# Optimization experiments

Measured on AMD Instinct MI355X. Metric: run time of the kernel, lower is better.

## Reference

```python
import jax, jax.numpy as jnp
import numpy as np

D = 256
NUMS_BC = np.array([10, 10, 10]) + 1
NUMS_SC = np.array([10, 10, 10, 10]) + 1
STARTS_BC = jnp.asarray(np.concatenate([[0], np.cumsum(NUMS_BC)[:-1]]))
STARTS_SC = jnp.asarray(np.concatenate([[0], np.cumsum(NUMS_SC)[:-1]]))


def _ln(x, g, b, eps=1e-5):
    mu = x.mean(-1, keepdims=True)
    var = ((x - mu) ** 2).mean(-1, keepdims=True)
    return (x - mu) * jax.lax.rsqrt(var + eps) * g + b


def _cate(x, table, starts, g, b):
    # x: [..., F] int; offset each feature column into its slice of the shared table
    idx = x + 1 + starts
    return _ln(table[idx].sum(-2), g, b)


def setup_inputs():
    key = jax.random.key(0)
    ks = jax.random.split(key, 12)
    B, N, E = 128, 48, 64
    s = 0.02
    return {
        "bond_index": jax.random.randint(ks[0], (B, 2, E), 0, N),
        "bond_feat_cate": jax.random.randint(ks[1], (B, E, 3), 0, 10),
        "bond_feat_float": jax.random.normal(ks[2], (B, E, 4)),
        "bond_mask": jnp.ones((B, E), jnp.float32),
        "structure_feat_cate": jax.random.randint(ks[3], (B, N, N, 4), 0, 10),
        "structure_feat_float": jax.random.normal(ks[4], (B, N, N, 8)),
        "table_bc": jax.random.normal(ks[5], (int(NUMS_BC.sum()), D)) * s,
        "ln_bc_g": jnp.ones((D,)), "ln_bc_b": jnp.zeros((D,)),
        "W_bf": jax.random.normal(ks[6], (4, D)) * s, "b_bf": jnp.zeros((D,)),
        "ln_bf_g": jnp.ones((D,)), "ln_bf_b": jnp.zeros((D,)),
        "table_sc": jax.random.normal(ks[7], (int(NUMS_SC.sum()), D)) * s,
        "ln_sc_g": jnp.ones((D,)), "ln_sc_b": jnp.zeros((D,)),
        "W_sf": jax.random.normal(ks[8], (8, D)) * s, "b_sf": jnp.zeros((D,)),
        "ln_sf_g": jnp.ones((D,)), "ln_sf_b": jnp.zeros((D,)),
        "virtual_edge_emb": jax.random.normal(ks[9], (D,)),
        "W_rev": jax.random.normal(ks[10], (D, D)) * s, "b_rev": jnp.zeros((D,)),
    }


def reference(bond_index, bond_feat_cate, bond_feat_float, bond_mask,
              structure_feat_cate, structure_feat_float,
              table_bc, ln_bc_g, ln_bc_b, W_bf, b_bf, ln_bf_g, ln_bf_b,
              table_sc, ln_sc_g, ln_sc_b, W_sf, b_sf, ln_sf_g, ln_sf_b,
              virtual_edge_emb, W_rev, b_rev):
    B, N = structure_feat_cate.shape[:2]
    M = N + 1  # +1 virtual node
    # per-bond embedding: cate-embed sum + linear float embed, both layernormed
    hb = _cate(bond_feat_cate, table_bc, STARTS_BC, ln_bc_g, ln_bc_b) \
         + _ln(bond_feat_float @ W_bf + b_bf, ln_bf_g, ln_bf_b)
    hb = hb * bond_mask[..., None]  # [B,E,D]
    # dense pairwise structure embedding for real-node block
    block = _cate(structure_feat_cate, table_sc, STARTS_SC, ln_sc_g, ln_sc_b) \
            + _ln(structure_feat_float @ W_sf + b_sf, ln_sf_g, ln_sf_b)  # [B,N,N,D]
    hs = jnp.zeros((B, M, M, hb.shape[-1]), hb.dtype)
    hs = hs.at[:, 0, :, :].set(virtual_edge_emb)
    hs = hs.at[:, :, 0, :].set(virtual_edge_emb)
    hs = hs.at[:, 1:, 1:, :].set(block)
    # scatter-add bond embeddings into (i,j) and reversed projection into (j,i)
    bi = bond_index + 1  # shift past virtual node
    br = jnp.arange(B)[:, None]
    hs = hs.at[br, bi[:, 0], bi[:, 1]].add(hb)
    hs = hs.at[br, bi[:, 1], bi[:, 0]].add(hb @ W_rev + b_rev)
    return hs
```

## Files before the change

### kernel.cpp

```cpp
#include <hip/hip_runtime.h>


#define DD 256
#define BB 128
#define NN 48
#define MM 49
#define EE 64

typedef unsigned long long u64;

__device__ __forceinline__ void wred2(float& s, float& q) {
#pragma unroll
    for (int off = 32; off > 0; off >>= 1) {
        s += __shfl_xor(s, off, 64);
        q += __shfl_xor(q, off, 64);
    }
}

__device__ __forceinline__ void ln4(float& x0, float& x1, float& x2, float& x3,
                                    const float* __restrict__ g,
                                    const float* __restrict__ bb, int d0) {
    float s = x0 + x1 + x2 + x3;
    float q = x0 * x0 + x1 * x1 + x2 * x2 + x3 * x3;
    wred2(s, q);
    float mu  = s * (1.0f / 256.0f);
    float var = q * (1.0f / 256.0f) - mu * mu;
    float rs  = rsqrtf(var + 1e-5f);
    float4 gv = *(const float4*)(g + d0);
    float4 bv = *(const float4*)(bb + d0);
    x0 = (x0 - mu) * rs * gv.x + bv.x;
    x1 = (x1 - mu) * rs * gv.y + bv.y;
    x2 = (x2 - mu) * rs * gv.z + bv.z;
    x3 = (x3 - mu) * rs * gv.w + bv.w;
}

__global__ __launch_bounds__(64) void k_masks(const int* __restrict__ bond_index,
                                              u64* __restrict__ maskA,
                                              u64* __restrict__ maskB) {
    const int b = blockIdx.x;
    const int e = threadIdx.x;
    const int bi0 = bond_index[b * 2 * EE + e];
    const int bi1 = bond_index[b * 2 * EE + EE + e];
    for (int i = 0; i < NN; ++i) {
        u64 mA = __ballot(bi0 == i);
        u64 mB = __ballot(bi1 == i);
        if (e == 0) {
            maskA[b * MM + i + 1] = mA;
            maskB[b * MM + i + 1] = mB;
        }
    }
}

__global__ __launch_bounds__(256) void k_bonds(
    const int* __restrict__ bfc, const float* __restrict__ bff,
    const float* __restrict__ bmask,
    const float* __restrict__ table_bc,
    const float* __restrict__ g_bc, const float* __restrict__ be_bc,
    const float* __restrict__ W_bf, const float* __restrict__ b_bf,
    const float* __restrict__ g_bf, const float* __restrict__ be_bf,
    const float* __restrict__ W_rev, const float* __restrict__ b_rev,
    float* __restrict__ hb_out, float* __restrict__ hbrev_out) {
    __shared__ float hb_lds[16][DD];
    const int blk   = blockIdx.x;
    const int b     = blk >> 2;
    const int group = blk & 3;
    const int tid   = threadIdx.x;
    const int wave  = tid >> 6;
    const int lane  = tid & 63;
    const int d0    = lane << 2;

#pragma unroll
    for (int q = 0; q < 4; ++q) {
        const int el = wave * 4 + q;
        const int be = b * EE + group * 16 + el;

        const int* fc = bfc + be * 3;
        const int i0 = fc[0] + 1;
        const int i1 = fc[1] + 12;
        const int i2 = fc[2] + 23;
        float4 r0 = *(const float4*)(table_bc + i0 * DD + d0);
        float4 r1 = *(const float4*)(table_bc + i1 * DD + d0);
        float4 r2 = *(const float4*)(table_bc + i2 * DD + d0);
        float x0 = r0.x + r1.x + r2.x;
        float x1 = r0.y + r1.y + r2.y;
        float x2 = r0.z + r1.z + r2.z;
        float x3 = r0.w + r1.w + r2.w;
        ln4(x0, x1, x2, x3, g_bc, be_bc, d0);

        float4 fr = *(const float4*)(bff + be * 4);
        float4 w0 = *(const float4*)(W_bf + 0 * DD + d0);
        float4 w1 = *(const float4*)(W_bf + 1 * DD + d0);
        float4 w2 = *(const float4*)(W_bf + 2 * DD + d0);
        float4 w3 = *(const float4*)(W_bf + 3 * DD + d0);
        float4 bb = *(const float4*)(b_bf + d0);
        float y0 = bb.x + fr.x * w0.x + fr.y * w1.x + fr.z * w2.x + fr.w * w3.x;
        float y1 = bb.y + fr.x * w0.y + fr.y * w1.y + fr.z * w2.y + fr.w * w3.y;
        float y2 = bb.z + fr.x * w0.z + fr.y * w1.z + fr.z * w2.z + fr.w * w3.z;
        float y3 = bb.w + fr.x * w0.w + fr.y * w1.w + fr.z * w2.w + fr.w * w3.w;
        ln4(y0, y1, y2, y3, g_bf, be_bf, d0);

        const float m = bmask[be];
        const float h0 = (x0 + y0) * m;
        const float h1 = (x1 + y1) * m;
        const float h2 = (x2 + y2) * m;
        const float h3 = (x3 + y3) * m;

        *(float4*)&hb_lds[el][d0] = make_float4(h0, h1, h2, h3);
        *(float4*)(hb_out + (size_t)be * DD + d0) = make_float4(h0, h1, h2, h3);
    }
    __syncthreads();

    const int d = tid;
    const float brv = b_rev[d];
    float acc[16];
#pragma unroll
    for (int e = 0; e < 16; ++e) acc[e] = brv;
    for (int k = 0; k < DD; k += 4) {
        const float w0 = W_rev[(k + 0) * DD + d];
        const float w1 = W_rev[(k + 1) * DD + d];
        const float w2 = W_rev[(k + 2) * DD + d];
        const float w3 = W_rev[(k + 3) * DD + d];
#pragma unroll
        for (int e = 0; e < 16; ++e) {
            float4 h = *(const float4*)&hb_lds[e][k];
            acc[e] += h.x * w0 + h.y * w1 + h.z * w2 + h.w * w3;
        }
    }
    const int be0 = b * EE + group * 16;
#pragma unroll
    for (int e = 0; e < 16; ++e) {
        hbrev_out[(size_t)(be0 + e) * DD + d] = acc[e];
    }
}

__global__ __launch_bounds__(256) void k_cells(
    const int* __restrict__ sfc, const float* __restrict__ sff,
    const float* __restrict__ table_sc,
    const float* __restrict__ g_sc, const float* __restrict__ be_sc,
    const float* __restrict__ W_sf, const float* __restrict__ b_sf,
    const float* __restrict__ g_sf, const float* __restrict__ be_sf,
    const float* __restrict__ vee,
    const u64* __restrict__ maskA, const u64* __restrict__ maskB,
    const float* __restrict__ hb, const float* __restrict__ hbrev,
    float* __restrict__ out) {
    const int wave = threadIdx.x >> 6;
    const int lane = threadIdx.x & 63;
    const int cell = blockIdx.x * 4 + wave;
    const int b = cell / (MM * MM);
    const int r = cell - b * (MM * MM);
    const int i = r / MM;
    const int j = r - i * MM;
    const int d0 = lane << 2;
    float* op = out + (size_t)cell * DD + d0;

    if (i == 0 || j == 0) {
        *(float4*)op = *(const float4*)(vee + d0);
        return;
    }

    const int ii = i - 1, jj = j - 1;
    const int cidx = (b * NN + ii) * NN + jj;

    const int4 fc = *(const int4*)(sfc + cidx * 4);
    float4 r0 = *(const float4*)(table_sc + (fc.x + 1)  * DD + d0);
    float4 r1 = *(const float4*)(table_sc + (fc.y + 12) * DD + d0);
    float4 r2 = *(const float4*)(table_sc + (fc.z + 23) * DD + d0);
    float4 r3 = *(const float4*)(table_sc + (fc.w + 34) * DD + d0);
    float x0 = r0.x + r1.x + r2.x + r3.x;
    float x1 = r0.y + r1.y + r2.y + r3.y;
    float x2 = r0.z + r1.z + r2.z + r3.z;
    float x3 = r0.w + r1.w + r2.w + r3.w;
    ln4(x0, x1, x2, x3, g_sc, be_sc, d0);

    const float* fp = sff + (size_t)cidx * 8;
    float4 fa = *(const float4*)fp;
    float4 fb = *(const float4*)(fp + 4);
    float f[8] = {fa.x, fa.y, fa.z, fa.w, fb.x, fb.y, fb.z, fb.w};
    float4 bbv = *(const float4*)(b_sf + d0);
    float y0 = bbv.x, y1 = bbv.y, y2 = bbv.z, y3 = bbv.w;
#pragma unroll
    for (int ff = 0; ff < 8; ++ff) {
        float4 wr = *(const float4*)(W_sf + ff * DD + d0);
        y0 += f[ff] * wr.x;
        y1 += f[ff] * wr.y;
        y2 += f[ff] * wr.z;
        y3 += f[ff] * wr.w;
    }
    ln4(y0, y1, y2, y3, g_sf, be_sf, d0);

    float h0 = x0 + y0, h1 = x1 + y1, h2 = x2 + y2, h3 = x3 + y3;

    const u64 mAi = maskA[b * MM + i];
    const u64 mBj = maskB[b * MM + j];
    const u64 mBi = maskB[b * MM + i];
    const u64 mAj = maskA[b * MM + j];
    u64 fwd = mAi & mBj;
    u64 rev = mBi & mAj;
    while (fwd) {
        const int e = __builtin_ctzll(fwd); fwd &= fwd - 1;
        float4 hv = *(const float4*)(hb + (size_t)(b * EE + e) * DD + d0);
        h0 += hv.x; h1 += hv.y; h2 += hv.z; h3 += hv.w;
    }
    while (rev) {
        const int e = __builtin_ctzll(rev); rev &= rev - 1;
        float4 hv = *(const float4*)(hbrev + (size_t)(b * EE + e) * DD + d0);
        h0 += hv.x; h1 += hv.y; h2 += hv.z; h3 += hv.w;
    }

    *(float4*)op = make_float4(h0, h1, h2, h3);
}

extern "C" void kernel_launch(void* const* d_in, const int* in_sizes, int n_in,
                              void* d_out, int out_size, void* d_ws, size_t ws_size,
                              hipStream_t stream) {
    const int*   bond_index = (const int*)d_in[0];
    const int*   bfc        = (const int*)d_in[1];
    const float* bff        = (const float*)d_in[2];
    const float* bmask      = (const float*)d_in[3];
    const int*   sfc        = (const int*)d_in[4];
    const float* sff        = (const float*)d_in[5];
    const float* table_bc   = (const float*)d_in[6];
    const float* g_bc       = (const float*)d_in[7];
    const float* be_bc      = (const float*)d_in[8];
    const float* W_bf       = (const float*)d_in[9];
    const float* b_bf       = (const float*)d_in[10];
    const float* g_bf       = (const float*)d_in[11];
    const float* be_bf      = (const float*)d_in[12];
    const float* table_sc   = (const float*)d_in[13];
    const float* g_sc       = (const float*)d_in[14];
    const float* be_sc      = (const float*)d_in[15];
    const float* W_sf       = (const float*)d_in[16];
    const float* b_sf       = (const float*)d_in[17];
    const float* g_sf       = (const float*)d_in[18];
    const float* be_sf      = (const float*)d_in[19];
    const float* vee        = (const float*)d_in[20];
    const float* W_rev      = (const float*)d_in[21];
    const float* b_rev      = (const float*)d_in[22];

    float* out = (float*)d_out;

    float* hb    = (float*)d_ws;
    float* hbrev = hb + (size_t)BB * EE * DD;
    u64*   maskA = (u64*)(hbrev + (size_t)BB * EE * DD);
    u64*   maskB = maskA + BB * MM;

    k_masks<<<BB, 64, 0, stream>>>(bond_index, maskA, maskB);
    k_bonds<<<BB * 4, 256, 0, stream>>>(bfc, bff, bmask, table_bc, g_bc, be_bc,
                                        W_bf, b_bf, g_bf, be_bf, W_rev, b_rev,
                                        hb, hbrev);
    k_cells<<<(BB * MM * MM) / 4, 256, 0, stream>>>(sfc, sff, table_sc, g_sc, be_sc,
                                                    W_sf, b_sf, g_sf, be_sf, vee,
                                                    maskA, maskB, hb, hbrev, out);
}
```

Before: 579.1 us.

## Precompute layernorm stats via Gram matrices and process seven cells per wave

```diff
diff --git a/kernel.cpp b/kernel.cpp
--- a/kernel.cpp
+++ b/kernel.cpp
@@ -6,8 +6,16 @@
 #define NN 48
 #define MM 49
 #define EE 64
+#define NSC 44
+#define NSF 9
 
 typedef unsigned long long u64;
+
+__device__ __forceinline__ float wredsum(float s) {
+#pragma unroll
+    for (int off = 32; off > 0; off >>= 1) s += __shfl_xor(s, off, 64);
+    return s;
+}
 
 __device__ __forceinline__ void wred2(float& s, float& q) {
 #pragma unroll
@@ -49,6 +57,87 @@
             maskB[b * MM + i + 1] = mB;
         }
     }
+}
+
+__global__ __launch_bounds__(256) void k_prep_means(const float* __restrict__ table_sc,
+                                                    const float* __restrict__ W_sf,
+                                                    const float* __restrict__ b_sf,
+                                                    float* __restrict__ m_sc,
+                                                    float* __restrict__ m_sf) {
+    const int w = (blockIdx.x * 256 + threadIdx.x) >> 6;
+    const int lane = threadIdx.x & 63;
+    if (w >= NSC + NSF) return;
+    const float* src = (w < NSC) ? table_sc + w * DD
+                     : (w == NSC) ? b_sf
+                                  : W_sf + (w - NSC - 1) * DD;
+    float4 v = *(const float4*)(src + lane * 4);
+    float s = wredsum(v.x + v.y + v.z + v.w);
+    if (lane == 0) {
+        if (w < NSC) m_sc[w] = s * (1.0f / 256.0f);
+        else         m_sf[w - NSC] = s * (1.0f / 256.0f);
+    }
+}
+
+__global__ __launch_bounds__(256) void k_prep_gram(const float* __restrict__ table_sc,
+                                                   const float* __restrict__ W_sf,
+                                                   const float* __restrict__ b_sf,
+                                                   const float* __restrict__ m_sc,
+                                                   const float* __restrict__ m_sf,
+                                                   float* __restrict__ G_sc,
+                                                   float* __restrict__ G_sf) {
+    const int w = (blockIdx.x * 256 + threadIdx.x) >> 6;
+    const int lane = threadIdx.x & 63;
+    if (w < NSC * NSC) {
+        const int a = w / NSC, c = w - a * NSC;
+        float4 va = *(const float4*)(table_sc + a * DD + lane * 4);
+        float4 vc = *(const float4*)(table_sc + c * DD + lane * 4);
+        float s = wredsum(va.x * vc.x + va.y * vc.y + va.z * vc.z + va.w * vc.w);
+        if (lane == 0) G_sc[w] = s * (1.0f / 256.0f) - m_sc[a] * m_sc[c];
+    } else if (w < NSC * NSC + NSF * NSF) {
+        const int p = w - NSC * NSC;
+        const int a = p / NSF, c = p - a * NSF;
+        const float* ra = (a == 0) ? b_sf : W_sf + (a - 1) * DD;
+        const float* rc = (c == 0) ? b_sf : W_sf + (c - 1) * DD;
+        float4 va = *(const float4*)(ra + lane * 4);
+        float4 vc = *(const float4*)(rc + lane * 4);
+        float s = wredsum(va.x * vc.x + va.y * vc.y + va.z * vc.z + va.w * vc.w);
+        if (lane == 0) G_sf[p] = s * (1.0f / 256.0f) - m_sf[a] * m_sf[c];
+    }
+}
+
+__global__ __launch_bounds__(256) void k_prep_cells(const int* __restrict__ sfc,
+                                                    const float* __restrict__ sff,
+                                                    const float* __restrict__ m_sc,
+                                                    const float* __restrict__ G_sc,
+                                                    const float* __restrict__ m_sf,
+                                                    const float* __restrict__ G_sf,
+                                                    float4* __restrict__ cellp) {
+    const int c = blockIdx.x * 256 + threadIdx.x;
+    const int4 fc = *(const int4*)(sfc + (size_t)c * 4);
+    int r[4] = {fc.x + 1, fc.y + 12, fc.z + 23, fc.w + 34};
+    float mu_c = m_sc[r[0]] + m_sc[r[1]] + m_sc[r[2]] + m_sc[r[3]];
+    float var_c = 0.f;
+#pragma unroll
+    for (int a = 0; a < 4; ++a)
+#pragma unroll
+        for (int d = 0; d < 4; ++d) var_c += G_sc[r[a] * NSC + r[d]];
+
+    float f[NSF];
+    f[0] = 1.f;
+    float4 fa = *(const float4*)(sff + (size_t)c * 8);
+    float4 fb = *(const float4*)(sff + (size_t)c * 8 + 4);
+    f[1] = fa.x; f[2] = fa.y; f[3] = fa.z; f[4] = fa.w;
+    f[5] = fb.x; f[6] = fb.y; f[7] = fb.z; f[8] = fb.w;
+    float mu_f = 0.f, var_f = 0.f;
+#pragma unroll
+    for (int k = 0; k < NSF; ++k) {
+        mu_f += f[k] * m_sf[k];
+        float t = 0.f;
+#pragma unroll
+        for (int l = 0; l < NSF; ++l) t += f[l] * G_sf[k * NSF + l];
+        var_f += f[k] * t;
+    }
+    cellp[c] = make_float4(mu_c, rsqrtf(var_c + 1e-5f), mu_f, rsqrtf(var_f + 1e-5f));
 }
 
 __global__ __launch_bounds__(256) void k_bonds(
@@ -142,72 +231,97 @@
     const float* __restrict__ vee,
     const u64* __restrict__ maskA, const u64* __restrict__ maskB,
     const float* __restrict__ hb, const float* __restrict__ hbrev,
+    const float4* __restrict__ cellp,
     float* __restrict__ out) {
-    const int wave = threadIdx.x >> 6;
     const int lane = threadIdx.x & 63;
-    const int cell = blockIdx.x * 4 + wave;
-    const int b = cell / (MM * MM);
-    const int r = cell - b * (MM * MM);
-    const int i = r / MM;
-    const int j = r - i * MM;
     const int d0 = lane << 2;
-    float* op = out + (size_t)cell * DD + d0;
-
-    if (i == 0 || j == 0) {
-        *(float4*)op = *(const float4*)(vee + d0);
+    const int wid = __builtin_amdgcn_readfirstlane(blockIdx.x * 4 + (threadIdx.x >> 6));
+    const int b  = wid / (MM * 7);
+    const int rr = wid - b * (MM * 7);
+    const int i  = rr / 7;
+    const int jc = rr - i * 7;
+    const int j0 = jc * 7;
+
+    const float4 veev = *(const float4*)(vee + d0);
+    float* orow = out + (((size_t)b * MM + i) * MM + j0) * DD + d0;
+
+    if (i == 0) {
+#pragma unroll
+        for (int jj = 0; jj < 7; ++jj) *(float4*)(orow + jj * DD) = veev;
         return;
     }
 
-    const int ii = i - 1, jj = j - 1;
-    const int cidx = (b * NN + ii) * NN + jj;
-
-    const int4 fc = *(const int4*)(sfc + cidx * 4);
-    float4 r0 = *(const float4*)(table_sc + (fc.x + 1)  * DD + d0);
-    float4 r1 = *(const float4*)(table_sc + (fc.y + 12) * DD + d0);
-    float4 r2 = *(const float4*)(table_sc + (fc.z + 23) * DD + d0);
-    float4 r3 = *(const float4*)(table_sc + (fc.w + 34) * DD + d0);
-    float x0 = r0.x + r1.x + r2.x + r3.x;
-    float x1 = r0.y + r1.y + r2.y + r3.y;
-    float x2 = r0.z + r1.z + r2.z + r3.z;
-    float x3 = r0.w + r1.w + r2.w + r3.w;
-    ln4(x0, x1, x2, x3, g_sc, be_sc, d0);
-
-    const float* fp = sff + (size_t)cidx * 8;
-    float4 fa = *(const float4*)fp;
-    float4 fb = *(const float4*)(fp + 4);
-    float f[8] = {fa.x, fa.y, fa.z, fa.w, fb.x, fb.y, fb.z, fb.w};
-    float4 bbv = *(const float4*)(b_sf + d0);
-    float y0 = bbv.x, y1 = bbv.y, y2 = bbv.z, y3 = bbv.w;
-#pragma unroll
-    for (int ff = 0; ff < 8; ++ff) {
-        float4 wr = *(const float4*)(W_sf + ff * DD + d0);
-        y0 += f[ff] * wr.x;
-        y1 += f[ff] * wr.y;
-        y2 += f[ff] * wr.z;
-        y3 += f[ff] * wr.w;
-    }
-    ln4(y0, y1, y2, y3, g_sf, be_sf, d0);
-
-    float h0 = x0 + y0, h1 = x1 + y1, h2 = x2 + y2, h3 = x3 + y3;
+    const float4 gsc  = *(const float4*)(g_sc + d0);
+    const float4 bsc  = *(const float4*)(be_sc + d0);
+    const float4 gsf  = *(const float4*)(g_sf + d0);
+    const float4 bsf2 = *(const float4*)(be_sf + d0);
+    const float4 bsf  = *(const float4*)(b_sf + d0);
+    float4 w[8];
+#pragma unroll
+    for (int k = 0; k < 8; ++k) w[k] = *(const float4*)(W_sf + k * DD + d0);
 
     const u64 mAi = maskA[b * MM + i];
-    const u64 mBj = maskB[b * MM + j];
     const u64 mBi = maskB[b * MM + i];
-    const u64 mAj = maskA[b * MM + j];
-    u64 fwd = mAi & mBj;
-    u64 rev = mBi & mAj;
-    while (fwd) {
-        const int e = __builtin_ctzll(fwd); fwd &= fwd - 1;
-        float4 hv = *(const float4*)(hb + (size_t)(b * EE + e) * DD + d0);
-        h0 += hv.x; h1 += hv.y; h2 += hv.z; h3 += hv.w;
-    }
-    while (rev) {
-        const int e = __builtin_ctzll(rev); rev &= rev - 1;
-        float4 hv = *(const float4*)(hbrev + (size_t)(b * EE + e) * DD + d0);
-        h0 += hv.x; h1 += hv.y; h2 += hv.z; h3 += hv.w;
-    }
-
-    *(float4*)op = make_float4(h0, h1, h2, h3);
+    const float* hbB = hb    + ((size_t)b * EE) * DD + d0;
+    const float* hrB = hbrev + ((size_t)b * EE) * DD + d0;
+    const int rowbase = (b * NN + (i - 1)) * NN - 1;
+
+    for (int jj = 0; jj < 7; ++jj) {
+        const int j = j0 + jj;
+        float* op = orow + jj * DD;
+        if (j == 0) { *(float4*)op = veev; continue; }
+
+        const int cidx = rowbase + j;
+        const int4 fc  = *(const int4*)(sfc + (size_t)cidx * 4);
+        const float4 p = cellp[cidx];
+        const float4 t0 = *(const float4*)(table_sc + (fc.x + 1)  * DD + d0);
+        const float4 t1 = *(const float4*)(table_sc + (fc.y + 12) * DD + d0);
+        const float4 t2 = *(const float4*)(table_sc + (fc.z + 23) * DD + d0);
+        const float4 t3 = *(const float4*)(table_sc + (fc.w + 34) * DD + d0);
+        const float4 fa  = *(const float4*)(sff + (size_t)cidx * 8);
+        const float4 fbv = *(const float4*)(sff + (size_t)cidx * 8 + 4);
+
+        float x0 = t0.x + t1.x + t2.x + t3.x;
+        float x1 = t0.y + t1.y + t2.y + t3.y;
+        float x2 = t0.z + t1.z + t2.z + t3.z;
+        float x3 = t0.w + t1.w + t2.w + t3.w;
+        x0 = (x0 - p.x) * p.y * gsc.x + bsc.x;
+        x1 = (x1 - p.x) * p.y * gsc.y + bsc.y;
+        x2 = (x2 - p.x) * p.y * gsc.z + bsc.z;
+        x3 = (x3 - p.x) * p.y * gsc.w + bsc.w;
+
+        float y0 = bsf.x + fa.x * w[0].x + fa.y * w[1].x + fa.z * w[2].x + fa.w * w[3].x
+                         + fbv.x * w[4].x + fbv.y * w[5].x + fbv.z * w[6].x + fbv.w * w[7].x;
+        float y1 = bsf.y + fa.x * w[0].y + fa.y * w[1].y + fa.z * w[2].y + fa.w * w[3].y
+                         + fbv.x * w[4].y + fbv.y * w[5].y + fbv.z * w[6].y + fbv.w * w[7].y;
+        float y2 = bsf.z + fa.x * w[0].z + fa.y * w[1].z + fa.z * w[2].z + fa.w * w[3].z
+                         + fbv.x * w[4].z + fbv.y * w[5].z + fbv.z * w[6].z + fbv.w * w[7].z;
+        float y3 = bsf.w + fa.x * w[0].w + fa.y * w[1].w + fa.z * w[2].w + fa.w * w[3].w
+                         + fbv.x * w[4].w + fbv.y * w[5].w + fbv.z * w[6].w + fbv.w * w[7].w;
+        y0 = (y0 - p.z) * p.w * gsf.x + bsf2.x;
+        y1 = (y1 - p.z) * p.w * gsf.y + bsf2.y;
+        y2 = (y2 - p.z) * p.w * gsf.z + bsf2.z;
+        y3 = (y3 - p.z) * p.w * gsf.w + bsf2.w;
+
+        float h0 = x0 + y0, h1 = x1 + y1, h2 = x2 + y2, h3 = x3 + y3;
+
+        const u64 mAj = maskA[b * MM + j];
+        const u64 mBj = maskB[b * MM + j];
+        u64 fwd = mAi & mBj;
+        u64 rev = mBi & mAj;
+        while (fwd) {
+            const int e = __builtin_ctzll(fwd); fwd &= fwd - 1;
+            float4 hv = *(const float4*)(hbB + (size_t)e * DD);
+            h0 += hv.x; h1 += hv.y; h2 += hv.z; h3 += hv.w;
+        }
+        while (rev) {
+            const int e = __builtin_ctzll(rev); rev &= rev - 1;
+            float4 hv = *(const float4*)(hrB + (size_t)e * DD);
+            h0 += hv.x; h1 += hv.y; h2 += hv.z; h3 += hv.w;
+        }
+
+        *(float4*)op = make_float4(h0, h1, h2, h3);
+    }
 }
 
 extern "C" void kernel_launch(void* const* d_in, const int* in_sizes, int n_in,
@@ -243,12 +357,22 @@
     float* hbrev = hb + (size_t)BB * EE * DD;
     u64*   maskA = (u64*)(hbrev + (size_t)BB * EE * DD);
     u64*   maskB = maskA + BB * MM;
+    float* m_sc  = (float*)(maskB + BB * MM);
+    float* G_sc  = m_sc + NSC;
+    float* m_sf  = G_sc + NSC * NSC;
+    float* G_sf  = m_sf + NSF;
+    float* endp  = G_sf + NSF * NSF;
+    float4* cellp = (float4*)(((unsigned long long)endp + 15ull) & ~15ull);
 
     k_masks<<<BB, 64, 0, stream>>>(bond_index, maskA, maskB);
+    k_prep_means<<<(NSC + NSF + 3) / 4, 256, 0, stream>>>(table_sc, W_sf, b_sf, m_sc, m_sf);
+    k_prep_gram<<<(NSC * NSC + NSF * NSF + 3) / 4, 256, 0, stream>>>(
+        table_sc, W_sf, b_sf, m_sc, m_sf, G_sc, G_sf);
+    k_prep_cells<<<(BB * NN * NN) / 256, 256, 0, stream>>>(sfc, sff, m_sc, G_sc, m_sf, G_sf, cellp);
     k_bonds<<<BB * 4, 256, 0, stream>>>(bfc, bff, bmask, table_bc, g_bc, be_bc,
                                         W_bf, b_bf, g_bf, be_bf, W_rev, b_rev,
                                         hb, hbrev);
-    k_cells<<<(BB * MM * MM) / 4, 256, 0, stream>>>(sfc, sff, table_sc, g_sc, be_sc,
-                                                    W_sf, b_sf, g_sf, be_sf, vee,
-                                                    maskA, maskB, hb, hbrev, out);
-}
+    k_cells<<<(BB * MM * 7) / 4, 256, 0, stream>>>(sfc, sff, table_sc, g_sc, be_sc,
+                                                   W_sf, b_sf, g_sf, be_sf, vee,
+                                                   maskA, maskB, hb, hbrev, cellp, out);
+}
```

After: 465.9 us. 1.24x faster.
